# Kernel tuning notes

Measured on AMD Instinct MI355X. Metric: run time of the kernel, lower is better.

The kernel has to match this reference:

```python
import jax, jax.numpy as jnp
import numpy as np

B, S, D, H = 4, 2048, 512, 8
DEPTH = D // H
EPS = 1e-6
NEG = -1e9


def _glorot(key, shape):
    fan_in, fan_out = shape[0], shape[1]
    limit = float(np.sqrt(6.0 / (fan_in + fan_out)))
    return jax.random.uniform(key, shape, jnp.float32, -limit, limit)


def setup_inputs() -> dict:
    key = jax.random.key(0)
    ks = jax.random.split(key, 10)
    return {
        "q": jax.random.normal(ks[0], (B, S, D), jnp.float32),
        "k": jax.random.normal(ks[1], (B, S, D), jnp.float32),
        "mask": jnp.zeros((B, 1, 1, S), jnp.float32),
        "wq": _glorot(ks[2], (D, D)),
        "wk": _glorot(ks[3], (D, D)),
        "wv": _glorot(ks[4], (D, D)),
        "wo": _glorot(ks[5], (D, D)),
        "w1": _glorot(ks[6], (D, D)),
        "b1": jnp.zeros((D,), jnp.float32),
        "w2": _glorot(ks[7], (D, D)),
        "b2": jnp.zeros((D,), jnp.float32),
        "g1": jnp.ones((D,), jnp.float32),
        "beta1": jnp.zeros((D,), jnp.float32),
        "g2": jnp.ones((D,), jnp.float32),
        "beta2": jnp.zeros((D,), jnp.float32),
    }


def _split_heads(x):
    b, s, _ = x.shape
    return x.reshape(b, s, H, DEPTH).transpose(0, 2, 1, 3)  # (B,H,S,depth)


def _layernorm(x, g, b):
    mu = jnp.mean(x, axis=-1, keepdims=True)
    var = jnp.var(x, axis=-1, keepdims=True)
    return (x - mu) * jax.lax.rsqrt(var + EPS) * g + b


def reference(q, k, mask, wq, wk, wv, wo, w1, b1, w2, b2, g1, beta1, g2, beta2):
    # Multi-head attention (q attends to k; v == k in TransformerLayer.call)
    qh = _split_heads(q @ wq)
    kh = _split_heads(k @ wk)
    vh = _split_heads(k @ wv)
    logits = jnp.einsum("bhqd,bhkd->bhqk", qh, kh) / jnp.sqrt(
        jnp.asarray(DEPTH, jnp.float32))
    logits = logits + mask * NEG
    attn = jax.nn.softmax(logits, axis=-1)
    ctx = jnp.einsum("bhqk,bhkd->bhqd", attn, vh)
    ctx = ctx.transpose(0, 2, 1, 3).reshape(q.shape[0], -1, D)
    attn_out = ctx @ wo
    # residual + LN1
    out1 = _layernorm(q + attn_out, g1, beta1)
    # pointwise FFN (d_model -> d_model -> d_model, leaky_relu alpha=0.2)
    h = jax.nn.leaky_relu(out1 @ w1 + b1, negative_slope=0.2)
    ffn_out = h @ w2 + b2
    # residual + LN2
    out2 = _layernorm(out1 + ffn_out, g2, beta2)
    return out2
```

## Files before the change

### kernel.cpp

```cpp
#include <hip/hip_runtime.h>
#include <hip/hip_bf16.h>
#include <math.h>

#define BB 4
#define SS 2048
#define DD 512
#define HH 8
#define DEPTH 64
#define NROWS (BB*SS)
#define LN_EPS 1e-6f

typedef __attribute__((ext_vector_type(8))) short bf16x8;
typedef __attribute__((ext_vector_type(4))) float f32x4;

static __device__ inline ushort f2bf(float f) {
    __hip_bfloat16 h = __float2bfloat16(f);
    return *reinterpret_cast<ushort*>(&h);
}
static __device__ inline float bf2f(ushort u) {
    __hip_bfloat16 h = *reinterpret_cast<__hip_bfloat16*>(&u);
    return __bfloat162float(h);
}

__global__ __launch_bounds__(256) void wtrans_kernel(
    const float* __restrict__ w0, const float* __restrict__ w1,
    const float* __restrict__ w2, const float* __restrict__ w3,
    const float* __restrict__ w4, const float* __restrict__ w5,
    ushort* __restrict__ wt)
{
    const float* W;
    switch (blockIdx.z) {
        case 0: W = w0; break; case 1: W = w1; break; case 2: W = w2; break;
        case 3: W = w3; break; case 4: W = w4; break; default: W = w5; break;
    }
    ushort* WT = wt + (size_t)blockIdx.z * DD * DD;

    __shared__ ushort t[64][72];
    const int kt = blockIdx.x * 64, nt = blockIdx.y * 64;
    const int tid = threadIdx.x;
    const int r = tid >> 2, cg = tid & 3;

    #pragma unroll
    for (int q = 0; q < 4; ++q) {
        float4 v = *reinterpret_cast<const float4*>(
            &W[(size_t)(kt + r) * DD + nt + cg * 16 + q * 4]);
        t[r][cg * 16 + q * 4 + 0] = f2bf(v.x);
        t[r][cg * 16 + q * 4 + 1] = f2bf(v.y);
        t[r][cg * 16 + q * 4 + 2] = f2bf(v.z);
        t[r][cg * 16 + q * 4 + 3] = f2bf(v.w);
    }
    __syncthreads();

    ushort tmp[16];
    #pragma unroll
    for (int i = 0; i < 16; ++i) tmp[i] = t[cg * 16 + i][r];
    *reinterpret_cast<bf16x8*>(&WT[(size_t)(nt + r) * DD + kt + cg * 16]) =
        *reinterpret_cast<bf16x8*>(&tmp[0]);
    *reinterpret_cast<bf16x8*>(&WT[(size_t)(nt + r) * DD + kt + cg * 16 + 8]) =
        *reinterpret_cast<bf16x8*>(&tmp[8]);
}

#define LDP 40

template<typename AT, typename CT, int ACT>
__global__ __launch_bounds__(256) void gemm2_kernel(
    const AT* __restrict__ A, const ushort* __restrict__ WT,
    const float* __restrict__ bias, CT* __restrict__ C)
{
    __shared__ __align__(16) ushort As[128 * LDP];
    __shared__ __align__(16) ushort Bs[128 * LDP];

    const int bm = blockIdx.y * 128;
    const int bn = blockIdx.x * 128;
    const int tid  = threadIdx.x;
    const int wave = tid >> 6;
    const int lane = tid & 63;
    const int wr = wave >> 1, wc = wave & 1;
    const int lm = lane & 15;
    const int kg = lane >> 4;

    f32x4 acc[4][4] = {};

    const int sr = tid >> 1;
    const int sh = tid & 1;

    for (int k0 = 0; k0 < DD; k0 += 32) {
        if constexpr (sizeof(AT) == 4) {
            const float* ga = (const float*)&A[(size_t)(bm + sr) * DD + k0 + sh * 16];
            ushort tmp[16];
            #pragma unroll
            for (int q = 0; q < 4; ++q) {
                float4 v = *reinterpret_cast<const float4*>(ga + q * 4);
                tmp[q*4+0] = f2bf(v.x); tmp[q*4+1] = f2bf(v.y);
                tmp[q*4+2] = f2bf(v.z); tmp[q*4+3] = f2bf(v.w);
            }
            *reinterpret_cast<bf16x8*>(&As[sr * LDP + sh * 16])     = *reinterpret_cast<bf16x8*>(&tmp[0]);
            *reinterpret_cast<bf16x8*>(&As[sr * LDP + sh * 16 + 8]) = *reinterpret_cast<bf16x8*>(&tmp[8]);
        } else {
            const ushort* ga = (const ushort*)&A[(size_t)(bm + sr) * DD + k0 + sh * 16];
            *reinterpret_cast<bf16x8*>(&As[sr * LDP + sh * 16]) =
                *reinterpret_cast<const bf16x8*>(ga);
            *reinterpret_cast<bf16x8*>(&As[sr * LDP + sh * 16 + 8]) =
                *reinterpret_cast<const bf16x8*>(ga + 8);
        }
        {
            const ushort* gw = &WT[(size_t)(bn + sr) * DD + k0 + sh * 16];
            *reinterpret_cast<bf16x8*>(&Bs[sr * LDP + sh * 16]) =
                *reinterpret_cast<const bf16x8*>(gw);
            *reinterpret_cast<bf16x8*>(&Bs[sr * LDP + sh * 16 + 8]) =
                *reinterpret_cast<const bf16x8*>(gw + 8);
        }
        __syncthreads();

        bf16x8 af[4], bfr[4];
        #pragma unroll
        for (int m = 0; m < 4; ++m)
            af[m] = *reinterpret_cast<const bf16x8*>(
                &As[(wr * 64 + m * 16 + lm) * LDP + kg * 8]);
        #pragma unroll
        for (int n = 0; n < 4; ++n)
            bfr[n] = *reinterpret_cast<const bf16x8*>(
                &Bs[(wc * 64 + n * 16 + lm) * LDP + kg * 8]);
        #pragma unroll
        for (int m = 0; m < 4; ++m)
            #pragma unroll
            for (int n = 0; n < 4; ++n)
                acc[m][n] = __builtin_amdgcn_mfma_f32_16x16x32_bf16(
                    af[m], bfr[n], acc[m][n], 0, 0, 0);
        __syncthreads();
    }

    #pragma unroll
    for (int m = 0; m < 4; ++m) {
        #pragma unroll
        for (int n = 0; n < 4; ++n) {
            const int col = bn + wc * 64 + n * 16 + lm;
            const float bv = bias ? bias[col] : 0.f;
            #pragma unroll
            for (int j = 0; j < 4; ++j) {
                const int row = bm + wr * 64 + m * 16 + kg * 4 + j;
                float v = acc[m][n][j] + bv;
                if (ACT == 1) v = (v > 0.f) ? v : 0.2f * v;
                if constexpr (sizeof(CT) == 4)
                    C[(size_t)row * DD + col] = v;
                else
                    C[(size_t)row * DD + col] = f2bf(v);
            }
        }
    }
}

#define AP 72
#define SP 68

__global__ __launch_bounds__(256) void attn_mfma_kernel(
    const ushort* __restrict__ qp, const ushort* __restrict__ kp,
    const ushort* __restrict__ vp, const float* __restrict__ mask,
    ushort* __restrict__ ctx)
{
    __shared__ __align__(16) ushort qs[64 * AP];
    __shared__ __align__(16) ushort ksh[64 * AP];
    __shared__ __align__(16) ushort vsT[64 * AP];
    __shared__ __align__(16) ushort pt[64 * AP];
    __shared__ __align__(16) float  st[64 * SP];
    __shared__ float crow[64];
    __shared__ float linv[64];

    const int qt = blockIdx.x, h = blockIdx.y, b = blockIdx.z;
    const int tid = threadIdx.x;
    const int wave = tid >> 6, lane = tid & 63;
    const int lm = lane & 15, kg = lane >> 4;
    const int r4 = tid >> 2;
    const int c4 = tid & 3;

    {
        const ushort* gq = &qp[(size_t)(b*SS + qt*64 + r4)*DD + h*DEPTH + c4*16];
        *reinterpret_cast<bf16x8*>(&qs[r4*AP + c4*16])     = *reinterpret_cast<const bf16x8*>(gq);
        *reinterpret_cast<bf16x8*>(&qs[r4*AP + c4*16 + 8]) = *reinterpret_cast<const bf16x8*>(gq + 8);
    }

    f32x4 acc[4] = {};
    float m_i = -1e30f, l_i = 0.f;

    for (int kt = 0; kt < SS/64; ++kt) {
        __syncthreads();

        {
            const size_t gb = (size_t)(b*SS + kt*64 + r4)*DD + h*DEPTH + c4*16;
            *reinterpret_cast<bf16x8*>(&ksh[r4*AP + c4*16])     = *reinterpret_cast<const bf16x8*>(&kp[gb]);
            *reinterpret_cast<bf16x8*>(&ksh[r4*AP + c4*16 + 8]) = *reinterpret_cast<const bf16x8*>(&kp[gb + 8]);

            ushort tv[16];
            *reinterpret_cast<bf16x8*>(&tv[0]) = *reinterpret_cast<const bf16x8*>(&vp[gb]);
            *reinterpret_cast<bf16x8*>(&tv[8]) = *reinterpret_cast<const bf16x8*>(&vp[gb + 8]);
            #pragma unroll
            for (int i = 0; i < 16; ++i) {
                const int dloc = c4*16 + i;
                const int e = (((r4>>3) ^ ((dloc>>3)&7)) << 3) | (r4 & 7);
                vsT[dloc*AP + e] = tv[i];
            }
        }
        __syncthreads();

        {
            f32x4 s[4] = {};
            #pragma unroll
            for (int ks_ = 0; ks_ < 2; ++ks_) {
                bf16x8 bfrag = *reinterpret_cast<const bf16x8*>(
                    &ksh[(wave*16 + lm)*AP + ks_*32 + kg*8]);
                #pragma unroll
                for (int m = 0; m < 4; ++m) {
                    bf16x8 afrag = *reinterpret_cast<const bf16x8*>(
                        &qs[(m*16 + lm)*AP + ks_*32 + kg*8]);
                    s[m] = __builtin_amdgcn_mfma_f32_16x16x32_bf16(
                        afrag, bfrag, s[m], 0, 0, 0);
                }
            }
            const int kcol = kt*64 + wave*16 + lm;
            const float mval = mask[b*SS + kcol] * (-1e9f);
            #pragma unroll
            for (int m = 0; m < 4; ++m)
                #pragma unroll
                for (int j = 0; j < 4; ++j)
                    st[(m*16 + kg*4 + j)*SP + wave*16 + lm] = s[m][j]*0.125f + mval;
        }
        __syncthreads();

        {
            float p[16];
            #pragma unroll
            for (int q = 0; q < 4; ++q) {
                float4 t = *reinterpret_cast<const float4*>(&st[r4*SP + c4*16 + q*4]);
                p[q*4+0] = t.x; p[q*4+1] = t.y; p[q*4+2] = t.z; p[q*4+3] = t.w;
            }
            float mt = p[0];
            #pragma unroll
            for (int i = 1; i < 16; ++i) mt = fmaxf(mt, p[i]);
            mt = fmaxf(mt, __shfl_xor(mt, 1));
            mt = fmaxf(mt, __shfl_xor(mt, 2));
            const float mnew = fmaxf(m_i, mt);
            const float corr = __expf(m_i - mnew);
            float sum = 0.f;
            ushort tmp[16];
            #pragma unroll
            for (int i = 0; i < 16; ++i) {
                float e = __expf(p[i] - mnew);
                sum += e;
                tmp[i] = f2bf(e);
            }
            sum += __shfl_xor(sum, 1);
            sum += __shfl_xor(sum, 2);
            l_i = l_i * corr + sum;
            m_i = mnew;
            *reinterpret_cast<bf16x8*>(&pt[r4*AP + c4*16])     = *reinterpret_cast<bf16x8*>(&tmp[0]);
            *reinterpret_cast<bf16x8*>(&pt[r4*AP + c4*16 + 8]) = *reinterpret_cast<bf16x8*>(&tmp[8]);
            if (c4 == 0) crow[r4] = corr;
        }
        __syncthreads();

        {
            #pragma unroll
            for (int m = 0; m < 4; ++m)
                #pragma unroll
                for (int j = 0; j < 4; ++j)
                    acc[m][j] *= crow[m*16 + kg*4 + j];

            const int dloc = wave*16 + lm;
            const int zz = (dloc >> 3) & 7;
            #pragma unroll
            for (int ks_ = 0; ks_ < 2; ++ks_) {
                const int chunk = (ks_*4 + kg) ^ zz;
                bf16x8 bfrag = *reinterpret_cast<const bf16x8*>(
                    &vsT[dloc*AP + chunk*8]);
                #pragma unroll
                for (int m = 0; m < 4; ++m) {
                    bf16x8 afrag = *reinterpret_cast<const bf16x8*>(
                        &pt[(m*16 + lm)*AP + ks_*32 + kg*8]);
                    acc[m] = __builtin_amdgcn_mfma_f32_16x16x32_bf16(
                        afrag, bfrag, acc[m], 0, 0, 0);
                }
            }
        }
    }

    if (c4 == 0) linv[r4] = 1.f / l_i;
    __syncthreads();

    {
        const int dloc = wave*16 + lm;
        #pragma unroll
        for (int m = 0; m < 4; ++m)
            #pragma unroll
            for (int j = 0; j < 4; ++j) {
                const int row = m*16 + kg*4 + j;
                ctx[(size_t)(b*SS + qt*64 + row)*DD + h*DEPTH + dloc] =
                    f2bf(acc[m][j] * linv[row]);
            }
    }
}

__global__ __launch_bounds__(256) void ln_kernel(
    const float* __restrict__ x, const float* __restrict__ res,
    const float* __restrict__ g, const float* __restrict__ bta,
    float* __restrict__ out, ushort* __restrict__ outb)
{
    const int row = blockIdx.x;
    const int tid = threadIdx.x;
    const size_t base = (size_t)row * DD + tid * 2;

    float2 xv = *reinterpret_cast<const float2*>(&x[base]);
    float2 rv = *reinterpret_cast<const float2*>(&res[base]);
    float v0 = xv.x + rv.x, v1 = xv.y + rv.y;

    float s = v0 + v1;
    float ss = v0 * v0 + v1 * v1;
    #pragma unroll
    for (int off = 32; off > 0; off >>= 1) {
        s  += __shfl_down(s, off);
        ss += __shfl_down(ss, off);
    }
    __shared__ float red[2][4];
    const int wid = tid >> 6, lane = tid & 63;
    if (lane == 0) { red[0][wid] = s; red[1][wid] = ss; }
    __syncthreads();
    const float tot = red[0][0] + red[0][1] + red[0][2] + red[0][3];
    const float tsq = red[1][0] + red[1][1] + red[1][2] + red[1][3];
    const float mu = tot * (1.f / DD);
    const float var = tsq * (1.f / DD) - mu * mu;
    const float rs = rsqrtf(var + LN_EPS);

    float2 gv = *reinterpret_cast<const float2*>(&g[tid * 2]);
    float2 bv = *reinterpret_cast<const float2*>(&bta[tid * 2]);
    float2 ov;
    ov.x = (v0 - mu) * rs * gv.x + bv.x;
    ov.y = (v1 - mu) * rs * gv.y + bv.y;
    *reinterpret_cast<float2*>(&out[base]) = ov;
    if (outb) {
        ushort2 ob; ob.x = f2bf(ov.x); ob.y = f2bf(ov.y);
        *reinterpret_cast<ushort2*>(&outb[base]) = ob;
    }
}

extern "C" void kernel_launch(void* const* d_in, const int* in_sizes, int n_in,
                              void* d_out, int out_size, void* d_ws, size_t ws_size,
                              hipStream_t stream)
{
    (void)in_sizes; (void)n_in; (void)out_size; (void)ws_size;
    const float* q     = (const float*)d_in[0];
    const float* k     = (const float*)d_in[1];
    const float* mask  = (const float*)d_in[2];
    const float* wq    = (const float*)d_in[3];
    const float* wk    = (const float*)d_in[4];
    const float* wv    = (const float*)d_in[5];
    const float* wo    = (const float*)d_in[6];
    const float* w1    = (const float*)d_in[7];
    const float* b1    = (const float*)d_in[8];
    const float* w2    = (const float*)d_in[9];
    const float* b2    = (const float*)d_in[10];
    const float* g1    = (const float*)d_in[11];
    const float* beta1 = (const float*)d_in[12];
    const float* g2    = (const float*)d_in[13];
    const float* beta2 = (const float*)d_in[14];
    float* out = (float*)d_out;

    uint8_t* base = (uint8_t*)d_ws;
    ushort* qpb = (ushort*)(base);
    ushort* kpb = (ushort*)(base + (8u  << 20));
    ushort* vpb = (ushort*)(base + (16u << 20));
    float*  ao  = (float*) (base + (24u << 20));
    ushort* o1b = (ushort*)(base + (40u << 20));
    ushort* wt  = (ushort*)(base + (48u << 20));
    ushort* wtq = wt;
    ushort* wtk = wt + 1u * DD * DD;
    ushort* wtv = wt + 2u * DD * DD;
    ushort* wto = wt + 3u * DD * DD;
    ushort* wt1 = wt + 4u * DD * DD;
    ushort* wt2 = wt + 5u * DD * DD;

    const dim3 blk(256);
    const dim3 ggrid(DD / 128, NROWS / 128);

    wtrans_kernel<<<dim3(8, 8, 6), blk, 0, stream>>>(wq, wk, wv, wo, w1, w2, wt);

    gemm2_kernel<float, ushort, 0><<<ggrid, blk, 0, stream>>>(q, wtq, nullptr, qpb);
    gemm2_kernel<float, ushort, 0><<<ggrid, blk, 0, stream>>>(k, wtk, nullptr, kpb);
    gemm2_kernel<float, ushort, 0><<<ggrid, blk, 0, stream>>>(k, wtv, nullptr, vpb);

    attn_mfma_kernel<<<dim3(SS / 64, HH, BB), blk, 0, stream>>>(qpb, kpb, vpb, mask, qpb);

    gemm2_kernel<ushort, float, 0><<<ggrid, blk, 0, stream>>>(qpb, wto, nullptr, ao);
    ln_kernel<<<dim3(NROWS), blk, 0, stream>>>(ao, q, g1, beta1, ao, o1b);

    gemm2_kernel<ushort, ushort, 1><<<ggrid, blk, 0, stream>>>(o1b, wt1, b1, kpb);
    gemm2_kernel<ushort, float, 0><<<ggrid, blk, 0, stream>>>(kpb, wt2, b2, out);

    ln_kernel<<<dim3(NROWS), blk, 0, stream>>>(out, ao, g2, beta2, out, nullptr);
}
```

Measured before the change: 389.0 us.

## Halve GEMM M-tile to 64 and batch Q/K/V projections into one launch

```diff
diff --git a/kernel.cpp b/kernel.cpp
--- a/kernel.cpp
+++ b/kernel.cpp
@@ -16,10 +16,6 @@
 static __device__ inline ushort f2bf(float f) {
     __hip_bfloat16 h = __float2bfloat16(f);
     return *reinterpret_cast<ushort*>(&h);
-}
-static __device__ inline float bf2f(ushort u) {
-    __hip_bfloat16 h = *reinterpret_cast<__hip_bfloat16*>(&u);
-    return __bfloat162float(h);
 }
 
 __global__ __launch_bounds__(256) void wtrans_kernel(
@@ -63,15 +59,11 @@
 #define LDP 40
 
 template<typename AT, typename CT, int ACT>
-__global__ __launch_bounds__(256) void gemm2_kernel(
+static __device__ __forceinline__ void gemm3_body(
     const AT* __restrict__ A, const ushort* __restrict__ WT,
-    const float* __restrict__ bias, CT* __restrict__ C)
-{
-    __shared__ __align__(16) ushort As[128 * LDP];
-    __shared__ __align__(16) ushort Bs[128 * LDP];
-
-    const int bm = blockIdx.y * 128;
-    const int bn = blockIdx.x * 128;
+    const float* __restrict__ bias, CT* __restrict__ C,
+    ushort* As, ushort* Bs, int bm, int bn)
+{
     const int tid  = threadIdx.x;
     const int wave = tid >> 6;
     const int lane = tid & 63;
@@ -79,50 +71,50 @@
     const int lm = lane & 15;
     const int kg = lane >> 4;
 
-    f32x4 acc[4][4] = {};
-
-    const int sr = tid >> 1;
-    const int sh = tid & 1;
+    f32x4 acc[2][4] = {};
+
+    const int ar = tid >> 2;
+    const int ac = (tid & 3) * 8;
+    const int br = tid >> 1;
+    const int bh = tid & 1;
 
     for (int k0 = 0; k0 < DD; k0 += 32) {
         if constexpr (sizeof(AT) == 4) {
-            const float* ga = (const float*)&A[(size_t)(bm + sr) * DD + k0 + sh * 16];
-            ushort tmp[16];
-            #pragma unroll
-            for (int q = 0; q < 4; ++q) {
-                float4 v = *reinterpret_cast<const float4*>(ga + q * 4);
-                tmp[q*4+0] = f2bf(v.x); tmp[q*4+1] = f2bf(v.y);
-                tmp[q*4+2] = f2bf(v.z); tmp[q*4+3] = f2bf(v.w);
-            }
-            *reinterpret_cast<bf16x8*>(&As[sr * LDP + sh * 16])     = *reinterpret_cast<bf16x8*>(&tmp[0]);
-            *reinterpret_cast<bf16x8*>(&As[sr * LDP + sh * 16 + 8]) = *reinterpret_cast<bf16x8*>(&tmp[8]);
+            const float* ga = (const float*)&A[(size_t)(bm + ar) * DD + k0 + ac];
+            float4 v0 = *reinterpret_cast<const float4*>(ga);
+            float4 v1 = *reinterpret_cast<const float4*>(ga + 4);
+            ushort tmp[8];
+            tmp[0] = f2bf(v0.x); tmp[1] = f2bf(v0.y);
+            tmp[2] = f2bf(v0.z); tmp[3] = f2bf(v0.w);
+            tmp[4] = f2bf(v1.x); tmp[5] = f2bf(v1.y);
+            tmp[6] = f2bf(v1.z); tmp[7] = f2bf(v1.w);
+            *reinterpret_cast<bf16x8*>(&As[ar * LDP + ac]) =
+                *reinterpret_cast<bf16x8*>(tmp);
         } else {
-            const ushort* ga = (const ushort*)&A[(size_t)(bm + sr) * DD + k0 + sh * 16];
-            *reinterpret_cast<bf16x8*>(&As[sr * LDP + sh * 16]) =
+            const ushort* ga = (const ushort*)&A[(size_t)(bm + ar) * DD + k0 + ac];
+            *reinterpret_cast<bf16x8*>(&As[ar * LDP + ac]) =
                 *reinterpret_cast<const bf16x8*>(ga);
-            *reinterpret_cast<bf16x8*>(&As[sr * LDP + sh * 16 + 8]) =
-                *reinterpret_cast<const bf16x8*>(ga + 8);
         }
         {
-            const ushort* gw = &WT[(size_t)(bn + sr) * DD + k0 + sh * 16];
-            *reinterpret_cast<bf16x8*>(&Bs[sr * LDP + sh * 16]) =
+            const ushort* gw = &WT[(size_t)(bn + br) * DD + k0 + bh * 16];
+            *reinterpret_cast<bf16x8*>(&Bs[br * LDP + bh * 16]) =
                 *reinterpret_cast<const bf16x8*>(gw);
-            *reinterpret_cast<bf16x8*>(&Bs[sr * LDP + sh * 16 + 8]) =
+            *reinterpret_cast<bf16x8*>(&Bs[br * LDP + bh * 16 + 8]) =
                 *reinterpret_cast<const bf16x8*>(gw + 8);
         }
         __syncthreads();
 
-        bf16x8 af[4], bfr[4];
+        bf16x8 af[2], bfr[4];
         #pragma unroll
-        for (int m = 0; m < 4; ++m)
+        for (int m = 0; m < 2; ++m)
             af[m] = *reinterpret_cast<const bf16x8*>(
-                &As[(wr * 64 + m * 16 + lm) * LDP + kg * 8]);
+                &As[(wr * 32 + m * 16 + lm) * LDP + kg * 8]);
         #pragma unroll
         for (int n = 0; n < 4; ++n)
             bfr[n] = *reinterpret_cast<const bf16x8*>(
                 &Bs[(wc * 64 + n * 16 + lm) * LDP + kg * 8]);
         #pragma unroll
-        for (int m = 0; m < 4; ++m)
+        for (int m = 0; m < 2; ++m)
             #pragma unroll
             for (int n = 0; n < 4; ++n)
                 acc[m][n] = __builtin_amdgcn_mfma_f32_16x16x32_bf16(
@@ -131,14 +123,14 @@
     }
 
     #pragma unroll
-    for (int m = 0; m < 4; ++m) {
+    for (int m = 0; m < 2; ++m) {
         #pragma unroll
         for (int n = 0; n < 4; ++n) {
             const int col = bn + wc * 64 + n * 16 + lm;
             const float bv = bias ? bias[col] : 0.f;
             #pragma unroll
             for (int j = 0; j < 4; ++j) {
-                const int row = bm + wr * 64 + m * 16 + kg * 4 + j;
+                const int row = bm + wr * 32 + m * 16 + kg * 4 + j;
                 float v = acc[m][n][j] + bv;
                 if (ACT == 1) v = (v > 0.f) ? v : 0.2f * v;
                 if constexpr (sizeof(CT) == 4)
@@ -148,6 +140,31 @@
             }
         }
     }
+}
+
+template<typename AT, typename CT, int ACT>
+__global__ __launch_bounds__(256) void gemm3_kernel(
+    const AT* __restrict__ A, const ushort* __restrict__ WT,
+    const float* __restrict__ bias, CT* __restrict__ C)
+{
+    __shared__ __align__(16) ushort As[64 * LDP];
+    __shared__ __align__(16) ushort Bs[128 * LDP];
+    gemm3_body<AT, CT, ACT>(A, WT, bias, C, As, Bs,
+                            blockIdx.y * 64, blockIdx.x * 128);
+}
+
+__global__ __launch_bounds__(256) void gemm3_proj_kernel(
+    const float* __restrict__ q, const float* __restrict__ k,
+    const ushort* __restrict__ wt, ushort* __restrict__ outb)
+{
+    __shared__ __align__(16) ushort As[64 * LDP];
+    __shared__ __align__(16) ushort Bs[128 * LDP];
+    const int z = blockIdx.z;
+    const float* A = (z == 0) ? q : k;
+    const ushort* WT = wt + (size_t)z * DD * DD;
+    ushort* C = outb + (size_t)z * NROWS * DD;
+    gemm3_body<float, ushort, 0>(A, WT, nullptr, C, As, Bs,
+                                 blockIdx.y * 64, blockIdx.x * 128);
 }
 
 #define AP 72
@@ -370,29 +387,24 @@
     float*  ao  = (float*) (base + (24u << 20));
     ushort* o1b = (ushort*)(base + (40u << 20));
     ushort* wt  = (ushort*)(base + (48u << 20));
-    ushort* wtq = wt;
-    ushort* wtk = wt + 1u * DD * DD;
-    ushort* wtv = wt + 2u * DD * DD;
     ushort* wto = wt + 3u * DD * DD;
     ushort* wt1 = wt + 4u * DD * DD;
     ushort* wt2 = wt + 5u * DD * DD;
 
     const dim3 blk(256);
-    const dim3 ggrid(DD / 128, NROWS / 128);
+    const dim3 ggrid(DD / 128, NROWS / 64);
 
     wtrans_kernel<<<dim3(8, 8, 6), blk, 0, stream>>>(wq, wk, wv, wo, w1, w2, wt);
 
-    gemm2_kernel<float, ushort, 0><<<ggrid, blk, 0, stream>>>(q, wtq, nullptr, qpb);
-    gemm2_kernel<float, ushort, 0><<<ggrid, blk, 0, stream>>>(k, wtk, nullptr, kpb);
-    gemm2_kernel<float, ushort, 0><<<ggrid, blk, 0, stream>>>(k, wtv, nullptr, vpb);
+    gemm3_proj_kernel<<<dim3(DD / 128, NROWS / 64, 3), blk, 0, stream>>>(q, k, wt, qpb);
 
     attn_mfma_kernel<<<dim3(SS / 64, HH, BB), blk, 0, stream>>>(qpb, kpb, vpb, mask, qpb);
 
-    gemm2_kernel<ushort, float, 0><<<ggrid, blk, 0, stream>>>(qpb, wto, nullptr, ao);
+    gemm3_kernel<ushort, float, 0><<<ggrid, blk, 0, stream>>>(qpb, wto, nullptr, ao);
     ln_kernel<<<dim3(NROWS), blk, 0, stream>>>(ao, q, g1, beta1, ao, o1b);
 
-    gemm2_kernel<ushort, ushort, 1><<<ggrid, blk, 0, stream>>>(o1b, wt1, b1, kpb);
-    gemm2_kernel<ushort, float, 0><<<ggrid, blk, 0, stream>>>(kpb, wt2, b2, out);
+    gemm3_kernel<ushort, ushort, 1><<<ggrid, blk, 0, stream>>>(o1b, wt1, b1, kpb);
+    gemm3_kernel<ushort, float, 0><<<ggrid, blk, 0, stream>>>(kpb, wt2, b2, out);
 
     ln_kernel<<<dim3(NROWS), blk, 0, stream>>>(out, ao, g2, beta2, out, nullptr);
 }
```

After: 338.4 us. 13.0% less time.
